# Kernel tuning notes

Measured on AMD Instinct MI355X. Metric: run time of the kernel, lower is better.

The kernel has to match this reference:

```python
import jax, jax.numpy as jnp
import numpy as np

D_MODEL = 1024
NUM_HEADS = 16


def setup_inputs() -> dict:
    key = jax.random.key(0)
    ks = jax.random.split(key, 5)
    B, S, D = 4, 2048, D_MODEL
    scale = 0.02  # realistic init scale so logits stay well-conditioned
    return {
        "x": jax.random.normal(ks[0], (B, S, D), dtype=jnp.float32),
        "Wq": jax.random.normal(ks[1], (D, D), dtype=jnp.float32) * scale,
        "Wk": jax.random.normal(ks[2], (D, D), dtype=jnp.float32) * scale,
        "Wv": jax.random.normal(ks[3], (D, D), dtype=jnp.float32) * scale,
        "Wo": jax.random.normal(ks[4], (D, D), dtype=jnp.float32) * scale,
    }


def reference(x, Wq, Wk, Wv, Wo):
    # x: (B, S, D). Weights are (d_out, d_in) as in the torch module.
    B, S, D = x.shape
    H = NUM_HEADS
    dk = D // H

    # Projections: einsum('oi,bli->blo') == x @ W.T
    q = jnp.einsum("oi,bsi->bso", Wq, x).reshape(B, S, H, dk).transpose(0, 2, 1, 3)
    k = jnp.einsum("oi,bsi->bso", Wk, x).reshape(B, S, H, dk).transpose(0, 2, 1, 3)
    v = jnp.einsum("oi,bsi->bso", Wv, x).reshape(B, S, H, dk).transpose(0, 2, 1, 3)

    # Scaled dot-product scores per head: (B, H, S, S)
    scores = jnp.einsum("bhqd,bhkd->bhqk", q, k) / jnp.sqrt(jnp.asarray(dk, x.dtype))

    # Causal mask (True = keep); masked entries get -inf (matches inf-subtraction)
    causal = jnp.tril(jnp.ones((S, S), dtype=bool))
    scores = jnp.where(causal, scores, -jnp.inf)

    attn = jax.nn.softmax(scores, axis=-1)

    out = jnp.einsum("bhqk,bhkd->bhqd", attn, v)  # (B, H, S, dk)
    out = out.transpose(0, 2, 1, 3).reshape(B, S, D)  # concat heads

    # Output projection: einsum('oi,bli->blo')
    return jnp.einsum("oi,bsi->bso", Wo, out)
```

## Files before the change

kernel.cpp:

```cpp
#include <hip/hip_runtime.h>
#include <hip/hip_bf16.h>

typedef unsigned short u16;
typedef __attribute__((ext_vector_type(8))) short short8;
typedef __attribute__((ext_vector_type(4))) float f32x4;

#if __has_builtin(__builtin_amdgcn_exp2f)
#define EXP2F(x) __builtin_amdgcn_exp2f(x)
#else
#define EXP2F(x) exp2f(x)
#endif

__device__ __forceinline__ float bf2f(u16 v) {
    union { unsigned u; float f; } c; c.u = ((unsigned)v) << 16; return c.f;
}
__device__ __forceinline__ u16 f2bf(float f) {
    union { float f; unsigned u; } c; c.f = f;
    unsigned r = c.u + 0x7fffu + ((c.u >> 16) & 1u);
    return (u16)(r >> 16);
}
__device__ __forceinline__ uint4 pack8(const float4 a, const float4 b) {
    uint4 r;
    r.x = (unsigned)f2bf(a.x) | ((unsigned)f2bf(a.y) << 16);
    r.y = (unsigned)f2bf(a.z) | ((unsigned)f2bf(a.w) << 16);
    r.z = (unsigned)f2bf(b.x) | ((unsigned)f2bf(b.y) << 16);
    r.w = (unsigned)f2bf(b.z) | ((unsigned)f2bf(b.w) << 16);
    return r;
}
__device__ __forceinline__ void gl_lds16(const u16* g, u16* l) {
    __builtin_amdgcn_global_load_lds((const __attribute__((address_space(1))) unsigned int*)g,
                                     (__attribute__((address_space(3))) unsigned int*)l, 16, 0, 0);
}

__global__ __launch_bounds__(256) void convert_all(const float* __restrict__ x,
                                                   const float* __restrict__ wq,
                                                   const float* __restrict__ wk,
                                                   const float* __restrict__ wv,
                                                   const float* __restrict__ wo,
                                                   u16* xb, u16* wqb, u16* wkb, u16* wvb, u16* wob) {
    size_t i8 = ((size_t)blockIdx.x * 256 + threadIdx.x) * 8;
    const float* src; u16* dst; size_t off;
    if (i8 < 8388608) { src = x; dst = xb; off = i8; }
    else {
        size_t idx = i8 - 8388608;
        int w = (int)(idx >> 20); off = idx & 1048575;
        src = (w == 0) ? wq : (w == 1) ? wk : (w == 2) ? wv : wo;
        dst = (w == 0) ? wqb : (w == 1) ? wkb : (w == 2) ? wvb : wob;
    }
    float4 a = *(const float4*)&src[off];
    float4 b = *(const float4*)&src[off + 4];
    *(uint4*)&dst[off] = pack8(a, b);
}

__device__ __forceinline__ void gemm_core(const u16* __restrict__ A, const u16* __restrict__ B,
                                          int m0, int n0, u16* As, u16* Bs, f32x4 acc[4][4]) {
    const int tid = threadIdx.x;
    const int wv = tid >> 6, lane = tid & 63, lr = lane & 15, quad = lane >> 4;
    const int srow = lane >> 3;
    const int scg  = (lane & 7) ^ srow;
    const int wm = (wv >> 1) * 64, wn = (wv & 1) * 64;

    for (int kt = 0; kt < 1024; kt += 64) {
        __syncthreads();
        #pragma unroll
        for (int t = 0; t < 4; ++t) {
            int r = wv * 32 + t * 8;
            gl_lds16(&A[(size_t)(m0 + r + srow) * 1024 + kt + scg * 8], &As[r * 64]);
            gl_lds16(&B[(size_t)(n0 + r + srow) * 1024 + kt + scg * 8], &Bs[r * 64]);
        }
        __syncthreads();
        #pragma unroll
        for (int c = 0; c < 2; ++c) {
            short8 af[4], bf[4];
            #pragma unroll
            for (int mi = 0; mi < 4; ++mi)
                af[mi] = *(const short8*)&As[(wm + mi * 16 + lr) * 64 + (((c * 4 + quad) ^ (lr & 7)) * 8)];
            #pragma unroll
            for (int ni = 0; ni < 4; ++ni)
                bf[ni] = *(const short8*)&Bs[(wn + ni * 16 + lr) * 64 + (((c * 4 + quad) ^ (lr & 7)) * 8)];
            #pragma unroll
            for (int mi = 0; mi < 4; ++mi)
                #pragma unroll
                for (int ni = 0; ni < 4; ++ni)
                    acc[mi][ni] = __builtin_amdgcn_mfma_f32_16x16x32_bf16(af[mi], bf[ni], acc[mi][ni], 0, 0, 0);
        }
    }
}

__global__ __launch_bounds__(256) void gemm_qkv(const u16* __restrict__ xb,
                                                const u16* __restrict__ wq,
                                                const u16* __restrict__ wk,
                                                const u16* __restrict__ wv,
                                                u16* __restrict__ Qb, u16* __restrict__ Kb,
                                                u16* __restrict__ Vtb) {
    __shared__ __align__(16) u16 As[8192];
    __shared__ __align__(16) u16 Bs[8192];
    const int bid = blockIdx.x;
    const int xcd = bid & 7;
    const int i   = bid >> 3;
    const int mi  = i & 7;
    const int nz  = i >> 3;
    const int z   = nz >> 3;
    const int nx  = nz & 7;
    const int mp  = xcd * 8 + mi;

    const u16* A; const u16* B; int m0, n0;
    if (z == 2) { A = wv; B = xb; m0 = nx * 128; n0 = mp * 128; }
    else        { A = xb; B = (z ? wk : wq); m0 = mp * 128; n0 = nx * 128; }

    f32x4 acc[4][4];
    #pragma unroll
    for (int a = 0; a < 4; ++a)
        #pragma unroll
        for (int j = 0; j < 4; ++j) acc[a][j] = 0;

    gemm_core(A, B, m0, n0, As, Bs, acc);

    const int lane = threadIdx.x & 63, lr = lane & 15, quad = lane >> 4;
    const int wv4 = threadIdx.x >> 6;
    const int wm = (wv4 >> 1) * 64, wn = (wv4 & 1) * 64;
    const float scale = (z == 0) ? 0.18033688f : 1.0f;
    #pragma unroll
    for (int mi2 = 0; mi2 < 4; ++mi2)
        #pragma unroll
        for (int ni = 0; ni < 4; ++ni)
            #pragma unroll
            for (int reg = 0; reg < 4; ++reg) {
                int row = m0 + wm + mi2 * 16 + quad * 4 + reg;
                int col = n0 + wn + ni * 16 + lr;
                u16 bv = f2bf(acc[mi2][ni][reg] * scale);
                if (z == 2) {
                    int bhh = (col >> 11) * 16 + (row >> 6);
                    Vtb[(size_t)bhh * 131072 + (size_t)(row & 63) * 2048 + (col & 2047)] = bv;
                } else {
                    int bhh = (row >> 11) * 16 + (col >> 6);
                    (z ? Kb : Qb)[(size_t)bhh * 131072 + (size_t)(row & 2047) * 64 + (col & 63)] = bv;
                }
            }
}

__global__ __launch_bounds__(256) void gemm_out(const u16* __restrict__ Ob,
                                                const u16* __restrict__ wo,
                                                float* __restrict__ C) {
    __shared__ __align__(16) u16 As[8192];
    __shared__ __align__(16) u16 Bs[8192];
    const int bid = blockIdx.x;
    const int xcd = bid & 7;
    const int i   = bid >> 3;
    const int mp  = xcd * 8 + (i & 7);
    const int m0  = mp * 128, n0 = (i >> 3) * 128;

    f32x4 acc[4][4];
    #pragma unroll
    for (int a = 0; a < 4; ++a)
        #pragma unroll
        for (int j = 0; j < 4; ++j) acc[a][j] = 0;

    gemm_core(Ob, wo, m0, n0, As, Bs, acc);

    const int lane = threadIdx.x & 63, lr = lane & 15, quad = lane >> 4;
    const int wv4 = threadIdx.x >> 6;
    const int wm = (wv4 >> 1) * 64, wn = (wv4 & 1) * 64;
    #pragma unroll
    for (int mi = 0; mi < 4; ++mi)
        #pragma unroll
        for (int ni = 0; ni < 4; ++ni)
            #pragma unroll
            for (int reg = 0; reg < 4; ++reg) {
                int row = m0 + wm + mi * 16 + quad * 4 + reg;
                int col = n0 + wn + ni * 16 + lr;
                C[(size_t)row * 1024 + col] = acc[mi][ni][reg];
            }
}

__global__ __launch_bounds__(512, 4) void attn_flash(const u16* __restrict__ Q,
                                                     const u16* __restrict__ K,
                                                     const u16* __restrict__ Vt,
                                                     u16* __restrict__ O) {
    __shared__ __align__(16) u16 Kbuf[2][4096];
    __shared__ __align__(16) u16 Vbuf[2][4096];
    __shared__ __align__(16) u16 Ps[8][2048];

    const int tid = threadIdx.x, wave = tid >> 6, lane = tid & 63;
    const int lr = lane & 15, quad = lane >> 4;
    const int bh = blockIdx.x & 63;
    const int p  = blockIdx.x >> 6;
    const int qt8 = (p < 4) ? (7 - p) : (p - 4);
    const int qbase = qt8 * 256 + wave * 32;
    const size_t base = (size_t)bh * 131072;

    const int srow = lane >> 3;
    const int scg  = (lane & 7) ^ srow;

    const short8 onesv = {0x3f80, 0x3f80, 0x3f80, 0x3f80, 0x3f80, 0x3f80, 0x3f80, 0x3f80};

    short8 qf[2][2];
    #pragma unroll
    for (int qmi = 0; qmi < 2; ++qmi)
        #pragma unroll
        for (int c = 0; c < 2; ++c)
            qf[qmi][c] = *(const short8*)&Q[base + (size_t)(qbase + qmi * 16 + lr) * 64 + c * 32 + quad * 8];

    f32x4 oacc[4][2];
    #pragma unroll
    for (int i = 0; i < 4; ++i) { oacc[i][0] = 0; oacc[i][1] = 0; }
    f32x4 lacc[2];
    lacc[0] = 0; lacc[1] = 0;

    const int jmax = 4 * qt8 + 3;
    const int r0 = wave * 8;

    gl_lds16(&K[base + (size_t)(r0 + srow) * 64 + scg * 8], &Kbuf[0][r0 * 64]);
    gl_lds16(&Vt[base + (size_t)(r0 + srow) * 2048 + scg * 8], &Vbuf[0][r0 * 64]);

    for (int j = 0; j <= jmax; ++j) {
        const int buf = j & 1;
        __syncthreads();
        if (j < jmax) {
            const int nb = buf ^ 1;
            gl_lds16(&K[base + (size_t)((j + 1) * 64 + r0 + srow) * 64 + scg * 8], &Kbuf[nb][r0 * 64]);
            gl_lds16(&Vt[base + (size_t)(r0 + srow) * 2048 + (j + 1) * 64 + scg * 8], &Vbuf[nb][r0 * 64]);
        }

        if (j * 64 <= qbase + 31) {
            f32x4 st[4][2];
            #pragma unroll
            for (int ni = 0; ni < 4; ++ni) { st[ni][0] = 0; st[ni][1] = 0; }
            __builtin_amdgcn_s_setprio(1);
            #pragma unroll
            for (int c = 0; c < 2; ++c) {
                short8 kf[4];
                #pragma unroll
                for (int ni = 0; ni < 4; ++ni)
                    kf[ni] = *(const short8*)&Kbuf[buf][(ni * 16 + lr) * 64 + (((c * 4 + quad) ^ (lr & 7)) * 8)];
                #pragma unroll
                for (int ni = 0; ni < 4; ++ni)
                    #pragma unroll
                    for (int qmi = 0; qmi < 2; ++qmi)
                        st[ni][qmi] = __builtin_amdgcn_mfma_f32_16x16x32_bf16(kf[ni], qf[qmi][c], st[ni][qmi], 0, 0, 0);
            }
            __builtin_amdgcn_s_setprio(0);

            if (j >= 4 * qt8) {
                #pragma unroll
                for (int ni = 0; ni < 4; ++ni)
                    #pragma unroll
                    for (int qmi = 0; qmi < 2; ++qmi)
                        #pragma unroll
                        for (int reg = 0; reg < 4; ++reg) {
                            int key = j * 64 + ni * 16 + quad * 4 + reg;
                            int q   = qbase + qmi * 16 + lr;
                            if (key > q) st[ni][qmi][reg] = -3.0e38f;
                        }
            }

            #pragma unroll
            for (int qmi = 0; qmi < 2; ++qmi) {
                #pragma unroll
                for (int ni = 0; ni < 4; ++ni) {
                    unsigned u0 = __float_as_uint(EXP2F(st[ni][qmi][0]));
                    unsigned u1 = __float_as_uint(EXP2F(st[ni][qmi][1]));
                    unsigned u2 = __float_as_uint(EXP2F(st[ni][qmi][2]));
                    unsigned u3 = __float_as_uint(EXP2F(st[ni][qmi][3]));
                    uint2 pk;
                    pk.x = __builtin_amdgcn_perm(u1, u0, 0x07060302);
                    pk.y = __builtin_amdgcn_perm(u3, u2, 0x07060302);
                    int g8 = ni * 2 + (quad >> 1);
                    *(uint2*)&Ps[wave][qmi * 1024 + lr * 64 + ((g8 ^ (lr & 7)) * 8 + (quad & 1) * 4)] = pk;
                }
            }

            __builtin_amdgcn_s_setprio(1);
            #pragma unroll
            for (int c = 0; c < 2; ++c) {
                short8 pf[2];
                #pragma unroll
                for (int qmi = 0; qmi < 2; ++qmi)
                    pf[qmi] = *(const short8*)&Ps[wave][qmi * 1024 + lr * 64 + (((c * 4 + quad) ^ (lr & 7)) * 8)];
                #pragma unroll
                for (int dmi = 0; dmi < 4; ++dmi) {
                    short8 vf = *(const short8*)&Vbuf[buf][(dmi * 16 + lr) * 64 + (((c * 4 + quad) ^ (lr & 7)) * 8)];
                    #pragma unroll
                    for (int qmi = 0; qmi < 2; ++qmi)
                        oacc[dmi][qmi] = __builtin_amdgcn_mfma_f32_16x16x32_bf16(vf, pf[qmi], oacc[dmi][qmi], 0, 0, 0);
                }
                #pragma unroll
                for (int qmi = 0; qmi < 2; ++qmi)
                    lacc[qmi] = __builtin_amdgcn_mfma_f32_16x16x32_bf16(onesv, pf[qmi], lacc[qmi], 0, 0, 0);
            }
            __builtin_amdgcn_s_setprio(0);
        }
    }

    const int b = bh >> 4, h = bh & 15;
    #pragma unroll
    for (int qmi = 0; qmi < 2; ++qmi) {
        float rl = 1.0f / lacc[qmi][0];
        int s = qbase + qmi * 16 + lr;
        #pragma unroll
        for (int dmi = 0; dmi < 4; ++dmi) {
            unsigned o0 = f2bf(oacc[dmi][qmi][0] * rl);
            unsigned o1 = f2bf(oacc[dmi][qmi][1] * rl);
            unsigned o2 = f2bf(oacc[dmi][qmi][2] * rl);
            unsigned o3 = f2bf(oacc[dmi][qmi][3] * rl);
            uint2 pk;
            pk.x = o0 | (o1 << 16);
            pk.y = o2 | (o3 << 16);
            *(uint2*)&O[((size_t)(b * 2048 + s)) * 1024 + h * 64 + dmi * 16 + quad * 4] = pk;
        }
    }
}

extern "C" void kernel_launch(void* const* d_in, const int* in_sizes, int n_in,
                              void* d_out, int out_size, void* d_ws, size_t ws_size,
                              hipStream_t stream) {
    const float* x  = (const float*)d_in[0];
    const float* Wq = (const float*)d_in[1];
    const float* Wk = (const float*)d_in[2];
    const float* Wv = (const float*)d_in[3];
    const float* Wo = (const float*)d_in[4];

    u16* xb  = (u16*)d_ws;
    u16* wqb = xb + 8388608;
    u16* wkb = wqb + 1048576;
    u16* wvb = wkb + 1048576;
    u16* wob = wvb + 1048576;
    u16* Qb  = wob + 1048576;
    u16* Kb  = Qb + 8388608;
    u16* Vtb = Kb + 8388608;
    u16* Ob  = xb;

    convert_all<<<6144, 256, 0, stream>>>(x, Wq, Wk, Wv, Wo, xb, wqb, wkb, wvb, wob);

    gemm_qkv<<<1536, 256, 0, stream>>>(xb, wqb, wkb, wvb, Qb, Kb, Vtb);

    attn_flash<<<512, 512, 0, stream>>>(Qb, Kb, Vtb, Ob);

    gemm_out<<<512, 256, 0, stream>>>(Ob, wob, (float*)d_out);
}
```

Before: 232.7 us.

## Rewrite projection GEMMs as 8-wave 128x256 tiles with triple-buffered async loads

Replaces the 4-wave 128x128 GEMM core with an 8-wave 128x256 tile core that triple-buffers K-slices in LDS and issues global-to-LDS loads for two steps ahead. It splits each step into two half-tile MFMA phases, each guarded by explicit vmcnt waits, s_barrier and setprio. The goal is to hide global load latency behind MFMA work and to raise reuse per block. In exchange it uses much more LDS per block (about 144KB), which limits occupancy to one block per CU. It also halves the grid sizes and depends on hand-tuned waitcnt counts being correct.

```diff
diff --git a/kernel.cpp b/kernel.cpp
--- a/kernel.cpp
+++ b/kernel.cpp
@@ -52,83 +52,158 @@
     *(uint4*)&dst[off] = pack8(a, b);
 }
 
-__device__ __forceinline__ void gemm_core(const u16* __restrict__ A, const u16* __restrict__ B,
-                                          int m0, int n0, u16* As, u16* Bs, f32x4 acc[4][4]) {
-    const int tid = threadIdx.x;
-    const int wv = tid >> 6, lane = tid & 63, lr = lane & 15, quad = lane >> 4;
-    const int srow = lane >> 3;
-    const int scg  = (lane & 7) ^ srow;
-    const int wm = (wv >> 1) * 64, wn = (wv & 1) * 64;
-
-    for (int kt = 0; kt < 1024; kt += 64) {
-        __syncthreads();
-        #pragma unroll
-        for (int t = 0; t < 4; ++t) {
-            int r = wv * 32 + t * 8;
-            gl_lds16(&A[(size_t)(m0 + r + srow) * 1024 + kt + scg * 8], &As[r * 64]);
-            gl_lds16(&B[(size_t)(n0 + r + srow) * 1024 + kt + scg * 8], &Bs[r * 64]);
-        }
-        __syncthreads();
-        #pragma unroll
-        for (int c = 0; c < 2; ++c) {
-            short8 af[4], bf[4];
-            #pragma unroll
-            for (int mi = 0; mi < 4; ++mi)
-                af[mi] = *(const short8*)&As[(wm + mi * 16 + lr) * 64 + (((c * 4 + quad) ^ (lr & 7)) * 8)];
+__device__ __forceinline__ void core8(const u16* __restrict__ A, const u16* __restrict__ B,
+                                      int m0, int n0, u16* As, u16* Bs, f32x4 acc[4][4]) {
+    const int tid = threadIdx.x, wid = tid >> 6, lane = tid & 63;
+    const int lr = lane & 15, quad = lane >> 4;
+    const int srow = lane >> 3, scg = (lane & 7) ^ srow;
+    const int wm = (wid >> 2) * 64, wn = (wid & 3) * 64;
+    const int lwr = wid * 8;
+
+    #pragma unroll
+    for (int kt = 0; kt < 2; ++kt) {
+        u16* Ad = As + kt * 8192;
+        u16* Bd = Bs + kt * 16384;
+        #pragma unroll
+        for (int c = 0; c < 4; ++c)
+            gl_lds16(&B[(size_t)(n0 + c * 64 + lwr + srow) * 1024 + kt * 64 + scg * 8],
+                     &Bd[c * 4096 + lwr * 64]);
+        #pragma unroll
+        for (int c = 0; c < 2; ++c)
+            gl_lds16(&A[(size_t)(m0 + c * 64 + lwr + srow) * 1024 + kt * 64 + scg * 8],
+                     &Ad[c * 4096 + lwr * 64]);
+    }
+
+    for (int it = 0; it < 16; ++it) {
+        const int cb = it % 3;
+        const int sb = (it + 2) % 3;
+        const u16* Ab = As + cb * 8192;
+        const u16* Bb = Bs + cb * 16384;
+        u16* An = As + sb * 8192;
+        u16* Bn = Bs + sb * 16384;
+        const int kn = it + 2;
+
+        if (it < 14) {
+            #pragma unroll
+            for (int c = 0; c < 3; ++c)
+                gl_lds16(&B[(size_t)(n0 + c * 64 + lwr + srow) * 1024 + kn * 64 + scg * 8],
+                         &Bn[c * 4096 + lwr * 64]);
+            asm volatile("s_waitcnt vmcnt(9)" ::: "memory");
+        } else if (it == 14) {
+            asm volatile("s_waitcnt vmcnt(6)" ::: "memory");
+        } else {
+            asm volatile("s_waitcnt vmcnt(0)" ::: "memory");
+        }
+        {
+            short8 af[2][2], bf[4][2];
+            #pragma unroll
+            for (int mi = 0; mi < 2; ++mi)
+                #pragma unroll
+                for (int ks = 0; ks < 2; ++ks)
+                    af[mi][ks] = *(const short8*)&Ab[(wm + mi * 16 + lr) * 64 + (((ks * 4 + quad) ^ (lr & 7)) * 8)];
             #pragma unroll
             for (int ni = 0; ni < 4; ++ni)
-                bf[ni] = *(const short8*)&Bs[(wn + ni * 16 + lr) * 64 + (((c * 4 + quad) ^ (lr & 7)) * 8)];
-            #pragma unroll
-            for (int mi = 0; mi < 4; ++mi)
+                #pragma unroll
+                for (int ks = 0; ks < 2; ++ks)
+                    bf[ni][ks] = *(const short8*)&Bb[(wn + ni * 16 + lr) * 64 + (((ks * 4 + quad) ^ (lr & 7)) * 8)];
+            __builtin_amdgcn_sched_barrier(0);
+            __builtin_amdgcn_s_barrier();
+            __builtin_amdgcn_s_setprio(1);
+            #pragma unroll
+            for (int mi = 0; mi < 2; ++mi)
                 #pragma unroll
                 for (int ni = 0; ni < 4; ++ni)
-                    acc[mi][ni] = __builtin_amdgcn_mfma_f32_16x16x32_bf16(af[mi], bf[ni], acc[mi][ni], 0, 0, 0);
-        }
-    }
-}
-
-__global__ __launch_bounds__(256) void gemm_qkv(const u16* __restrict__ xb,
+                    #pragma unroll
+                    for (int ks = 0; ks < 2; ++ks)
+                        acc[mi][ni] = __builtin_amdgcn_mfma_f32_16x16x32_bf16(af[mi][ks], bf[ni][ks], acc[mi][ni], 0, 0, 0);
+            __builtin_amdgcn_s_setprio(0);
+            __builtin_amdgcn_sched_barrier(0);
+            __builtin_amdgcn_s_barrier();
+        }
+        if (it < 14) {
+            gl_lds16(&B[(size_t)(n0 + 192 + lwr + srow) * 1024 + kn * 64 + scg * 8],
+                     &Bn[12288 + lwr * 64]);
+            #pragma unroll
+            for (int c = 0; c < 2; ++c)
+                gl_lds16(&A[(size_t)(m0 + c * 64 + lwr + srow) * 1024 + kn * 64 + scg * 8],
+                         &An[c * 4096 + lwr * 64]);
+        }
+        {
+            short8 af[2][2], bf[4][2];
+            #pragma unroll
+            for (int mi = 0; mi < 2; ++mi)
+                #pragma unroll
+                for (int ks = 0; ks < 2; ++ks)
+                    af[mi][ks] = *(const short8*)&Ab[(wm + (mi + 2) * 16 + lr) * 64 + (((ks * 4 + quad) ^ (lr & 7)) * 8)];
+            #pragma unroll
+            for (int ni = 0; ni < 4; ++ni)
+                #pragma unroll
+                for (int ks = 0; ks < 2; ++ks)
+                    bf[ni][ks] = *(const short8*)&Bb[(wn + ni * 16 + lr) * 64 + (((ks * 4 + quad) ^ (lr & 7)) * 8)];
+            __builtin_amdgcn_sched_barrier(0);
+            __builtin_amdgcn_s_barrier();
+            __builtin_amdgcn_s_setprio(1);
+            #pragma unroll
+            for (int mi = 0; mi < 2; ++mi)
+                #pragma unroll
+                for (int ni = 0; ni < 4; ++ni)
+                    #pragma unroll
+                    for (int ks = 0; ks < 2; ++ks)
+                        acc[mi + 2][ni] = __builtin_amdgcn_mfma_f32_16x16x32_bf16(af[mi][ks], bf[ni][ks], acc[mi + 2][ni], 0, 0, 0);
+            __builtin_amdgcn_s_setprio(0);
+            __builtin_amdgcn_sched_barrier(0);
+            __builtin_amdgcn_s_barrier();
+        }
+    }
+}
+
+__global__ __launch_bounds__(512) void gemm_qkv(const u16* __restrict__ xb,
                                                 const u16* __restrict__ wq,
                                                 const u16* __restrict__ wk,
                                                 const u16* __restrict__ wv,
                                                 u16* __restrict__ Qb, u16* __restrict__ Kb,
                                                 u16* __restrict__ Vtb) {
-    __shared__ __align__(16) u16 As[8192];
-    __shared__ __align__(16) u16 Bs[8192];
+    __shared__ __align__(16) u16 As[24576];
+    __shared__ __align__(16) u16 Bs[49152];
     const int bid = blockIdx.x;
     const int xcd = bid & 7;
     const int i   = bid >> 3;
-    const int mi  = i & 7;
-    const int nz  = i >> 3;
-    const int z   = nz >> 3;
-    const int nx  = nz & 7;
-    const int mp  = xcd * 8 + mi;
-
-    const u16* A; const u16* B; int m0, n0;
-    if (z == 2) { A = wv; B = xb; m0 = nx * 128; n0 = mp * 128; }
-    else        { A = xb; B = (z ? wk : wq); m0 = mp * 128; n0 = nx * 128; }
+    const u16* A; const u16* B; int m0, n0, z;
+    if (i < 64) {
+        z = i >> 5;
+        const int local = i & 31;
+        m0 = (xcd * 8 + (local & 7)) * 128;
+        n0 = (local >> 3) * 256;
+        A = xb; B = z ? wk : wq;
+    } else {
+        z = 2;
+        const int j = i - 64;
+        m0 = (j & 7) * 128;
+        n0 = (xcd * 4 + (j >> 3)) * 256;
+        A = wv; B = xb;
+    }
 
     f32x4 acc[4][4];
     #pragma unroll
     for (int a = 0; a < 4; ++a)
         #pragma unroll
-        for (int j = 0; j < 4; ++j) acc[a][j] = 0;
-
-    gemm_core(A, B, m0, n0, As, Bs, acc);
+        for (int b = 0; b < 4; ++b) acc[a][b] = 0;
+
+    core8(A, B, m0, n0, As, Bs, acc);
 
     const int lane = threadIdx.x & 63, lr = lane & 15, quad = lane >> 4;
-    const int wv4 = threadIdx.x >> 6;
-    const int wm = (wv4 >> 1) * 64, wn = (wv4 & 1) * 64;
+    const int wid = threadIdx.x >> 6;
+    const int wm = (wid >> 2) * 64, wn = (wid & 3) * 64;
     const float scale = (z == 0) ? 0.18033688f : 1.0f;
     #pragma unroll
-    for (int mi2 = 0; mi2 < 4; ++mi2)
+    for (int mi = 0; mi < 4; ++mi)
         #pragma unroll
         for (int ni = 0; ni < 4; ++ni)
             #pragma unroll
             for (int reg = 0; reg < 4; ++reg) {
-                int row = m0 + wm + mi2 * 16 + quad * 4 + reg;
+                int row = m0 + wm + mi * 16 + quad * 4 + reg;
                 int col = n0 + wn + ni * 16 + lr;
-                u16 bv = f2bf(acc[mi2][ni][reg] * scale);
+                u16 bv = f2bf(acc[mi][ni][reg] * scale);
                 if (z == 2) {
                     int bhh = (col >> 11) * 16 + (row >> 6);
                     Vtb[(size_t)bhh * 131072 + (size_t)(row & 63) * 2048 + (col & 2047)] = bv;
@@ -139,28 +214,28 @@
             }
 }
 
-__global__ __launch_bounds__(256) void gemm_out(const u16* __restrict__ Ob,
+__global__ __launch_bounds__(512) void gemm_out(const u16* __restrict__ Ob,
                                                 const u16* __restrict__ wo,
                                                 float* __restrict__ C) {
-    __shared__ __align__(16) u16 As[8192];
-    __shared__ __align__(16) u16 Bs[8192];
+    __shared__ __align__(16) u16 As[24576];
+    __shared__ __align__(16) u16 Bs[49152];
     const int bid = blockIdx.x;
     const int xcd = bid & 7;
     const int i   = bid >> 3;
-    const int mp  = xcd * 8 + (i & 7);
-    const int m0  = mp * 128, n0 = (i >> 3) * 128;
+    const int m0  = (xcd * 8 + (i & 7)) * 128;
+    const int n0  = (i >> 3) * 256;
 
     f32x4 acc[4][4];
     #pragma unroll
     for (int a = 0; a < 4; ++a)
         #pragma unroll
-        for (int j = 0; j < 4; ++j) acc[a][j] = 0;
-
-    gemm_core(Ob, wo, m0, n0, As, Bs, acc);
+        for (int b = 0; b < 4; ++b) acc[a][b] = 0;
+
+    core8(Ob, wo, m0, n0, As, Bs, acc);
 
     const int lane = threadIdx.x & 63, lr = lane & 15, quad = lane >> 4;
-    const int wv4 = threadIdx.x >> 6;
-    const int wm = (wv4 >> 1) * 64, wn = (wv4 & 1) * 64;
+    const int wid = threadIdx.x >> 6;
+    const int wm = (wid >> 2) * 64, wn = (wid & 3) * 64;
     #pragma unroll
     for (int mi = 0; mi < 4; ++mi)
         #pragma unroll
@@ -332,9 +407,9 @@
 
     convert_all<<<6144, 256, 0, stream>>>(x, Wq, Wk, Wv, Wo, xb, wqb, wkb, wvb, wob);
 
-    gemm_qkv<<<1536, 256, 0, stream>>>(xb, wqb, wkb, wvb, Qb, Kb, Vtb);
+    gemm_qkv<<<768, 512, 0, stream>>>(xb, wqb, wkb, wvb, Qb, Kb, Vtb);
 
     attn_flash<<<512, 512, 0, stream>>>(Qb, Kb, Vtb, Ob);
 
-    gemm_out<<<512, 256, 0, stream>>>(Ob, wob, (float*)d_out);
-}
+    gemm_out<<<256, 512, 0, stream>>>(Ob, wob, (float*)d_out);
+}
```

After: 275.9 us. 1.19x slower.

## Share A tile across two B tiles in dual-output 512-thread GEMMs

Applied to the files above, without the earlier changes.

Replaces the 128x128 single-output GEMM core with a dual-output core in which 8 waves share one A tile in LDS against two B tiles. The QKV GEMM now computes Q and K together from the same x tile, and V over two adjacent column blocks. The output GEMM covers a 128x256 tile per block. This roughly halves A-tile global loads and the number of blocks, at the cost of more LDS per block (48KB), fewer blocks in flight (768 and 256), and a possible occupancy or tail-effect loss.

```diff
diff --git a/kernel.cpp b/kernel.cpp
--- a/kernel.cpp
+++ b/kernel.cpp
@@ -52,124 +52,156 @@
     *(uint4*)&dst[off] = pack8(a, b);
 }
 
-__device__ __forceinline__ void gemm_core(const u16* __restrict__ A, const u16* __restrict__ B,
-                                          int m0, int n0, u16* As, u16* Bs, f32x4 acc[4][4]) {
+__device__ __forceinline__ void core_dual(const u16* __restrict__ A,
+                                          const u16* __restrict__ B0,
+                                          const u16* __restrict__ B1,
+                                          int m0, int n0a, int n0b,
+                                          u16* As, u16* Bs0, u16* Bs1,
+                                          f32x4 acc0[2][4], f32x4 acc1[2][4]) {
     const int tid = threadIdx.x;
-    const int wv = tid >> 6, lane = tid & 63, lr = lane & 15, quad = lane >> 4;
+    const int wid = tid >> 6, lane = tid & 63, lr = lane & 15, quad = lane >> 4;
     const int srow = lane >> 3;
     const int scg  = (lane & 7) ^ srow;
-    const int wm = (wv >> 1) * 64, wn = (wv & 1) * 64;
+    const int wm = (wid >> 1) * 32, wn = (wid & 1) * 64;
+    const int r0 = wid * 16;
 
     for (int kt = 0; kt < 1024; kt += 64) {
         __syncthreads();
         #pragma unroll
-        for (int t = 0; t < 4; ++t) {
-            int r = wv * 32 + t * 8;
-            gl_lds16(&A[(size_t)(m0 + r + srow) * 1024 + kt + scg * 8], &As[r * 64]);
-            gl_lds16(&B[(size_t)(n0 + r + srow) * 1024 + kt + scg * 8], &Bs[r * 64]);
+        for (int h = 0; h < 2; ++h) {
+            int r = r0 + h * 8;
+            gl_lds16(&A [(size_t)(m0  + r + srow) * 1024 + kt + scg * 8], &As [r * 64]);
+            gl_lds16(&B0[(size_t)(n0a + r + srow) * 1024 + kt + scg * 8], &Bs0[r * 64]);
+            gl_lds16(&B1[(size_t)(n0b + r + srow) * 1024 + kt + scg * 8], &Bs1[r * 64]);
         }
         __syncthreads();
         #pragma unroll
         for (int c = 0; c < 2; ++c) {
-            short8 af[4], bf[4];
-            #pragma unroll
-            for (int mi = 0; mi < 4; ++mi)
+            short8 af[2], bf[4];
+            #pragma unroll
+            for (int mi = 0; mi < 2; ++mi)
                 af[mi] = *(const short8*)&As[(wm + mi * 16 + lr) * 64 + (((c * 4 + quad) ^ (lr & 7)) * 8)];
             #pragma unroll
             for (int ni = 0; ni < 4; ++ni)
-                bf[ni] = *(const short8*)&Bs[(wn + ni * 16 + lr) * 64 + (((c * 4 + quad) ^ (lr & 7)) * 8)];
-            #pragma unroll
-            for (int mi = 0; mi < 4; ++mi)
-                #pragma unroll
-                for (int ni = 0; ni < 4; ++ni)
-                    acc[mi][ni] = __builtin_amdgcn_mfma_f32_16x16x32_bf16(af[mi], bf[ni], acc[mi][ni], 0, 0, 0);
-        }
-    }
-}
-
-__global__ __launch_bounds__(256) void gemm_qkv(const u16* __restrict__ xb,
-                                                const u16* __restrict__ wq,
-                                                const u16* __restrict__ wk,
-                                                const u16* __restrict__ wv,
-                                                u16* __restrict__ Qb, u16* __restrict__ Kb,
-                                                u16* __restrict__ Vtb) {
-    __shared__ __align__(16) u16 As[8192];
-    __shared__ __align__(16) u16 Bs[8192];
+                bf[ni] = *(const short8*)&Bs0[(wn + ni * 16 + lr) * 64 + (((c * 4 + quad) ^ (lr & 7)) * 8)];
+            #pragma unroll
+            for (int mi = 0; mi < 2; ++mi)
+                #pragma unroll
+                for (int ni = 0; ni < 4; ++ni)
+                    acc0[mi][ni] = __builtin_amdgcn_mfma_f32_16x16x32_bf16(af[mi], bf[ni], acc0[mi][ni], 0, 0, 0);
+            #pragma unroll
+            for (int ni = 0; ni < 4; ++ni)
+                bf[ni] = *(const short8*)&Bs1[(wn + ni * 16 + lr) * 64 + (((c * 4 + quad) ^ (lr & 7)) * 8)];
+            #pragma unroll
+            for (int mi = 0; mi < 2; ++mi)
+                #pragma unroll
+                for (int ni = 0; ni < 4; ++ni)
+                    acc1[mi][ni] = __builtin_amdgcn_mfma_f32_16x16x32_bf16(af[mi], bf[ni], acc1[mi][ni], 0, 0, 0);
+        }
+    }
+}
+
+__global__ __launch_bounds__(512, 4) void gemm_qkv(const u16* __restrict__ xb,
+                                                   const u16* __restrict__ wq,
+                                                   const u16* __restrict__ wk,
+                                                   const u16* __restrict__ wv,
+                                                   u16* __restrict__ Qb, u16* __restrict__ Kb,
+                                                   u16* __restrict__ Vtb) {
+    __shared__ __align__(16) u16 As [8192];
+    __shared__ __align__(16) u16 Bs0[8192];
+    __shared__ __align__(16) u16 Bs1[8192];
+    const int bid = blockIdx.x;
+
+    f32x4 acc0[2][4], acc1[2][4];
+    #pragma unroll
+    for (int a = 0; a < 2; ++a)
+        #pragma unroll
+        for (int b = 0; b < 4; ++b) { acc0[a][b] = 0; acc1[a][b] = 0; }
+
+    const int lane = threadIdx.x & 63, lr = lane & 15, quad = lane >> 4;
+    const int wid = threadIdx.x >> 6;
+    const int wm = (wid >> 1) * 32, wn = (wid & 1) * 64;
+
+    if (bid < 512) {
+        const int xcd = bid & 7;
+        const int i   = bid >> 3;
+        const int m0  = (xcd * 8 + (i & 7)) * 128;
+        const int n0  = (i >> 3) * 128;
+        core_dual(xb, wq, wk, m0, n0, n0, As, Bs0, Bs1, acc0, acc1);
+        #pragma unroll
+        for (int mi = 0; mi < 2; ++mi)
+            #pragma unroll
+            for (int ni = 0; ni < 4; ++ni)
+                #pragma unroll
+                for (int reg = 0; reg < 4; ++reg) {
+                    int row = m0 + wm + mi * 16 + quad * 4 + reg;
+                    int col = n0 + wn + ni * 16 + lr;
+                    int bhh = (row >> 11) * 16 + (col >> 6);
+                    size_t o = (size_t)bhh * 131072 + (size_t)(row & 2047) * 64 + (col & 63);
+                    Qb[o] = f2bf(acc0[mi][ni][reg] * 0.18033688f);
+                    Kb[o] = f2bf(acc1[mi][ni][reg]);
+                }
+    } else {
+        const int t   = bid - 512;
+        const int xcd = t & 7;
+        const int j   = t >> 3;
+        const int m0  = (j & 7) * 128;
+        const int np  = xcd * 4 + (j >> 3);
+        const int n0a = np * 256, n0b = np * 256 + 128;
+        core_dual(wv, xb, xb, m0, n0a, n0b, As, Bs0, Bs1, acc0, acc1);
+        #pragma unroll
+        for (int half = 0; half < 2; ++half) {
+            const int nb = half ? n0b : n0a;
+            #pragma unroll
+            for (int mi = 0; mi < 2; ++mi)
+                #pragma unroll
+                for (int ni = 0; ni < 4; ++ni)
+                    #pragma unroll
+                    for (int reg = 0; reg < 4; ++reg) {
+                        int row = m0 + wm + mi * 16 + quad * 4 + reg;
+                        int col = nb + wn + ni * 16 + lr;
+                        int bhh = (col >> 11) * 16 + (row >> 6);
+                        float v = half ? acc1[mi][ni][reg] : acc0[mi][ni][reg];
+                        Vtb[(size_t)bhh * 131072 + (size_t)(row & 63) * 2048 + (col & 2047)] = f2bf(v);
+                    }
+        }
+    }
+}
+
+__global__ __launch_bounds__(512, 4) void gemm_out(const u16* __restrict__ Ob,
+                                                   const u16* __restrict__ wo,
+                                                   float* __restrict__ C) {
+    __shared__ __align__(16) u16 As [8192];
+    __shared__ __align__(16) u16 Bs0[8192];
+    __shared__ __align__(16) u16 Bs1[8192];
     const int bid = blockIdx.x;
     const int xcd = bid & 7;
     const int i   = bid >> 3;
-    const int mi  = i & 7;
-    const int nz  = i >> 3;
-    const int z   = nz >> 3;
-    const int nx  = nz & 7;
-    const int mp  = xcd * 8 + mi;
-
-    const u16* A; const u16* B; int m0, n0;
-    if (z == 2) { A = wv; B = xb; m0 = nx * 128; n0 = mp * 128; }
-    else        { A = xb; B = (z ? wk : wq); m0 = mp * 128; n0 = nx * 128; }
-
-    f32x4 acc[4][4];
-    #pragma unroll
-    for (int a = 0; a < 4; ++a)
-        #pragma unroll
-        for (int j = 0; j < 4; ++j) acc[a][j] = 0;
-
-    gemm_core(A, B, m0, n0, As, Bs, acc);
+    const int m0  = (xcd * 8 + (i & 7)) * 128;
+    const int np  = i >> 3;
+    const int n0a = np * 256, n0b = np * 256 + 128;
+
+    f32x4 acc0[2][4], acc1[2][4];
+    #pragma unroll
+    for (int a = 0; a < 2; ++a)
+        #pragma unroll
+        for (int b = 0; b < 4; ++b) { acc0[a][b] = 0; acc1[a][b] = 0; }
+
+    core_dual(Ob, wo, wo, m0, n0a, n0b, As, Bs0, Bs1, acc0, acc1);
 
     const int lane = threadIdx.x & 63, lr = lane & 15, quad = lane >> 4;
-    const int wv4 = threadIdx.x >> 6;
-    const int wm = (wv4 >> 1) * 64, wn = (wv4 & 1) * 64;
-    const float scale = (z == 0) ? 0.18033688f : 1.0f;
-    #pragma unroll
-    for (int mi2 = 0; mi2 < 4; ++mi2)
-        #pragma unroll
-        for (int ni = 0; ni < 4; ++ni)
-            #pragma unroll
-            for (int reg = 0; reg < 4; ++reg) {
-                int row = m0 + wm + mi2 * 16 + quad * 4 + reg;
-                int col = n0 + wn + ni * 16 + lr;
-                u16 bv = f2bf(acc[mi2][ni][reg] * scale);
-                if (z == 2) {
-                    int bhh = (col >> 11) * 16 + (row >> 6);
-                    Vtb[(size_t)bhh * 131072 + (size_t)(row & 63) * 2048 + (col & 2047)] = bv;
-                } else {
-                    int bhh = (row >> 11) * 16 + (col >> 6);
-                    (z ? Kb : Qb)[(size_t)bhh * 131072 + (size_t)(row & 2047) * 64 + (col & 63)] = bv;
-                }
-            }
-}
-
-__global__ __launch_bounds__(256) void gemm_out(const u16* __restrict__ Ob,
-                                                const u16* __restrict__ wo,
-                                                float* __restrict__ C) {
-    __shared__ __align__(16) u16 As[8192];
-    __shared__ __align__(16) u16 Bs[8192];
-    const int bid = blockIdx.x;
-    const int xcd = bid & 7;
-    const int i   = bid >> 3;
-    const int mp  = xcd * 8 + (i & 7);
-    const int m0  = mp * 128, n0 = (i >> 3) * 128;
-
-    f32x4 acc[4][4];
-    #pragma unroll
-    for (int a = 0; a < 4; ++a)
-        #pragma unroll
-        for (int j = 0; j < 4; ++j) acc[a][j] = 0;
-
-    gemm_core(Ob, wo, m0, n0, As, Bs, acc);
-
-    const int lane = threadIdx.x & 63, lr = lane & 15, quad = lane >> 4;
-    const int wv4 = threadIdx.x >> 6;
-    const int wm = (wv4 >> 1) * 64, wn = (wv4 & 1) * 64;
-    #pragma unroll
-    for (int mi = 0; mi < 4; ++mi)
+    const int wid = threadIdx.x >> 6;
+    const int wm = (wid >> 1) * 32, wn = (wid & 1) * 64;
+    #pragma unroll
+    for (int mi = 0; mi < 2; ++mi)
         #pragma unroll
         for (int ni = 0; ni < 4; ++ni)
             #pragma unroll
             for (int reg = 0; reg < 4; ++reg) {
                 int row = m0 + wm + mi * 16 + quad * 4 + reg;
-                int col = n0 + wn + ni * 16 + lr;
-                C[(size_t)row * 1024 + col] = acc[mi][ni][reg];
+                int col = wn + ni * 16 + lr;
+                C[(size_t)row * 1024 + n0a + col] = acc0[mi][ni][reg];
+                C[(size_t)row * 1024 + n0b + col] = acc1[mi][ni][reg];
             }
 }
 
@@ -332,9 +364,9 @@
 
     convert_all<<<6144, 256, 0, stream>>>(x, Wq, Wk, Wv, Wo, xb, wqb, wkb, wvb, wob);
 
-    gemm_qkv<<<1536, 256, 0, stream>>>(xb, wqb, wkb, wvb, Qb, Kb, Vtb);
+    gemm_qkv<<<768, 512, 0, stream>>>(xb, wqb, wkb, wvb, Qb, Kb, Vtb);
 
     attn_flash<<<512, 512, 0, stream>>>(Qb, Kb, Vtb, Ob);
 
-    gemm_out<<<512, 256, 0, stream>>>(Ob, wob, (float*)d_out);
-}
+    gemm_out<<<256, 512, 0, stream>>>(Ob, wob, (float*)d_out);
+}
```

New measurement: 231.0 us. No clear change (-0.7%).
